# Optimization experiments

Hardware: AMD Instinct MI355X
Metric: run time of the kernel (lower is better)

Reference implementation:

```python
import jax, jax.numpy as jnp
import numpy as np
from jax import lax

H = 50; W = 50; C = 512; A = 9; P = 3; K = 2048; NC = 20
DIN = C * P * P  # 4608, flattened ROI-pooled feature


def _conv(x, w, b):
    # x [N,H,W,Cin], w [kh,kw,Cin,Cout]
    return lax.conv_general_dilated(x, w, (1, 1), 'SAME',
                                    dimension_numbers=('NHWC', 'HWIO', 'NHWC')) + b


def _roi_align(feat, boxes):
    # feat [H,W,C]; boxes [K,4] = (x1,x2,y1,y2) in feature-map coords -> [K,P,P,C]
    Hf, Wf, _ = feat.shape
    t = (jnp.arange(P, dtype=feat.dtype) + 0.5) / P
    xs = boxes[:, 0:1] + (boxes[:, 1:2] - boxes[:, 0:1]) * t  # [K,P]
    ys = boxes[:, 2:3] + (boxes[:, 3:4] - boxes[:, 2:3]) * t  # [K,P]
    x0f = jnp.floor(xs); y0f = jnp.floor(ys)
    fx = (xs - x0f)[:, None, :, None]  # [K,1,P,1]
    fy = (ys - y0f)[:, :, None, None]  # [K,P,1,1]
    x0 = jnp.clip(x0f.astype(jnp.int32), 0, Wf - 1); x1i = jnp.clip(x0 + 1, 0, Wf - 1)
    y0 = jnp.clip(y0f.astype(jnp.int32), 0, Hf - 1); y1i = jnp.clip(y0 + 1, 0, Hf - 1)

    def g(yi, xi):  # [K,P],[K,P] -> [K,P,P,C]
        return feat[yi[:, :, None], xi[:, None, :]]

    return (g(y0, x0) * (1 - fy) * (1 - fx) + g(y0, x1i) * (1 - fy) * fx
            + g(y1i, x0) * fy * (1 - fx) + g(y1i, x1i) * fy * fx)


def setup_inputs() -> dict:
    key = jax.random.key(0)
    ks = jax.random.split(key, 16)

    def w(k, shape, fan_in):
        return jax.random.normal(k, shape, jnp.float32) / np.float32(np.sqrt(fan_in))

    return {
        'features': jax.random.normal(ks[0], (1, H, W, C), jnp.float32),
        'labels': jax.random.randint(ks[1], (NC,), 0, 2, dtype=jnp.int32),
        'rpn_w': w(ks[2], (2, 2, C, C), 4 * C), 'rpn_b': jnp.zeros((C,), jnp.float32),
        'cls_w': w(ks[3], (1, 1, C, A), C), 'cls_b': jnp.zeros((A,), jnp.float32),
        'reg_w': w(ks[4], (1, 1, C, 4 * A), C), 'reg_b': jnp.zeros((4 * A,), jnp.float32),
        'fc6_w': w(ks[5], (DIN, 9216), DIN), 'fc6_b': jnp.zeros((9216,), jnp.float32),
        'fc7_w': w(ks[6], (9216, 4096), 9216), 'fc7_b': jnp.zeros((4096,), jnp.float32),
        'fc8c_w': w(ks[7], (4096, NC), 4096), 'fc8c_b': jnp.zeros((NC,), jnp.float32),
        'fc8d_w': w(ks[8], (4096, NC), 4096), 'fc8d_b': jnp.zeros((NC,), jnp.float32),
    }


def reference(features, labels, rpn_w, rpn_b, cls_w, cls_b, reg_w, reg_b,
              fc6_w, fc6_b, fc7_w, fc7_b, fc8c_w, fc8c_b, fc8d_w, fc8d_b):
    # RPN head
    x = jax.nn.relu(_conv(features, rpn_w, rpn_b))
    obj = jax.nn.sigmoid(_conv(x, cls_w, cls_b))  # [1,H,W,A] objectness
    reg = _conv(x, reg_w, reg_b)
    # Objectness filtering: fixed-size top-K replaces dynamic threshold filter
    _, idx = lax.top_k(obj.reshape(-1), K)
    raw = reg.reshape(-1, 4)[idx]                 # [K,4]
    s = jax.nn.sigmoid(raw)
    Wd = jnp.float32(W); Hd = jnp.float32(H)
    x1 = s[:, 0] * (Wd - 2.0); x2 = x1 + 1.0 + s[:, 1] * (Wd - 1.0 - x1)
    y1 = s[:, 2] * (Hd - 2.0); y2 = y1 + 1.0 + s[:, 3] * (Hd - 1.0 - y1)
    # original slices feature map with integer coords -> non-differentiable
    boxes = lax.stop_gradient(jnp.stack([x1, x2, y1, y2], axis=1))  # [K,4]
    # Per-ROI pooling (vectorized ROI-align)
    pooled = _roi_align(features[0], boxes).reshape(K, -1)  # [K,DIN]
    # FC trunk + two-stream WSDDN head
    h = jax.nn.relu(pooled @ fc6_w + fc6_b)
    h = jax.nn.relu(h @ fc7_w + fc7_b)
    c = jax.nn.softmax(h @ fc8c_w + fc8c_b, axis=0)  # softmax over regions
    d = jax.nn.softmax(h @ fc8d_w + fc8d_b, axis=1)  # softmax over classes
    scores = c * d                                   # [K,NC]
    output = jnp.clip(jnp.sum(scores, axis=0), 0.0, 1.0)  # [NC]
    return output, scores, boxes
```

## Files before the change

kernel.cpp:

```cpp
#include <hip/hip_runtime.h>
#include <math.h>


#define HN 50
#define WN 50
#define CN 512
#define AN 9
#define KTOP 2048
#define NCL 20
#define NOBJ 22500

typedef unsigned short ushort_t;
typedef __attribute__((ext_vector_type(8))) short short8;
typedef __attribute__((ext_vector_type(4))) float floatx4;

__device__ __forceinline__ ushort_t bf16_rne(float f) {
    unsigned int u = __float_as_uint(f);
    unsigned int r = (u + 0x7FFFu + ((u >> 16) & 1u)) >> 16;
    return (ushort_t)r;
}

__device__ __forceinline__ void gl_lds16(const void* g, void* l) {
    __builtin_amdgcn_global_load_lds(
        (const __attribute__((address_space(1))) unsigned int*)g,
        (__attribute__((address_space(3))) unsigned int*)l, 16, 0, 0);
}

__launch_bounds__(256)
__global__ void conv_chain_kernel(const float* __restrict__ feat,
                                  const float* __restrict__ rpnw,
                                  const float* __restrict__ rpnb,
                                  float* __restrict__ x32)
{
    __shared__ float xs[16 * 512];
    const int tid = threadIdx.x;
    const int hwBase = blockIdx.x * 4;
    const int co = blockIdx.y * 256 + tid;

    for (int t = tid; t < 16 * 512; t += 256) {
        int slot = t >> 9, c = t & 511;
        int hwL = slot >> 2, tap = slot & 3;
        int hw = hwBase + hwL;
        int h = hw / WN, w = hw % WN;
        int hy = h + (tap >> 1), wx = w + (tap & 1);
        float v = 0.f;
        if (hy < HN && wx < WN) v = feat[(size_t)(hy * WN + wx) * CN + c];
        xs[t] = v;
    }
    __syncthreads();

    float acc[4][4];
#pragma unroll
    for (int i = 0; i < 4; i++)
#pragma unroll
        for (int t = 0; t < 4; t++) acc[i][t] = 0.f;

    for (int c = 0; c < CN; c++) {
        float wv0 = rpnw[(size_t)(0 * CN + c) * CN + co];
        float wv1 = rpnw[(size_t)(1 * CN + c) * CN + co];
        float wv2 = rpnw[(size_t)(2 * CN + c) * CN + co];
        float wv3 = rpnw[(size_t)(3 * CN + c) * CN + co];
#pragma unroll
        for (int i = 0; i < 4; i++) {
            acc[i][0] = fmaf(xs[(i * 4 + 0) * 512 + c], wv0, acc[i][0]);
            acc[i][1] = fmaf(xs[(i * 4 + 1) * 512 + c], wv1, acc[i][1]);
            acc[i][2] = fmaf(xs[(i * 4 + 2) * 512 + c], wv2, acc[i][2]);
            acc[i][3] = fmaf(xs[(i * 4 + 3) * 512 + c], wv3, acc[i][3]);
        }
    }
    float b = rpnb[co];
#pragma unroll
    for (int i = 0; i < 4; i++) {
        float v = ((acc[i][0] + acc[i][1]) + acc[i][2]) + acc[i][3];
        v = v + b;
        v = v > 0.f ? v : 0.f;
        x32[(size_t)(hwBase + i) * CN + co] = v;
    }
}

__launch_bounds__(256)
__global__ void obj_chain_kernel(const float* __restrict__ x32,
                                 const float* __restrict__ clsw,
                                 const float* __restrict__ clsb,
                                 float* __restrict__ key)
{
    int i = blockIdx.x * 256 + threadIdx.x;
    if (i >= NOBJ) return;
    int hw = i / AN, a = i % AN;
    const float* xr = x32 + (size_t)hw * CN;
    float acc = 0.f;
    for (int c = 0; c < CN; c++) acc = fmaf(xr[c], clsw[c * AN + a], acc);
    float l32 = acc + clsb[a];
    float s32 = (float)(1.0 / (1.0 + exp(-(double)l32)));
    key[i] = s32;
}

__launch_bounds__(256)
__global__ void topk_count_kernel(const float* __restrict__ key, int* __restrict__ cnt)
{
    __shared__ float ch[2048];
    int tid = threadIdx.x;
    int j0 = blockIdx.y * 2048;
    for (int t = tid; t < 2048; t += 256) {
        int jg = j0 + t;
        ch[t] = (jg < NOBJ) ? key[jg] : -1.0f;
    }
    int i = blockIdx.x * 256 + tid;
    float vi = (i < NOBJ) ? key[i] : 2.0f;
    __syncthreads();
    int c = 0;
    for (int t = 0; t < 2048; t++) {
        float vj = ch[t];
        int jg = j0 + t;
        c += (vj > vi || (vj == vi && jg < i)) ? 1 : 0;
    }
    if (i < NOBJ && c) atomicAdd(&cnt[i], c);
}

__launch_bounds__(256)
__global__ void topk_scatter_kernel(const int* __restrict__ cnt, int* __restrict__ sorted)
{
    int i = blockIdx.x * 256 + threadIdx.x;
    if (i < NOBJ) {
        int r = cnt[i];
        if (r < KTOP) sorted[r] = i;
    }
}

__launch_bounds__(256)
__global__ void boxes_kernel(const int* __restrict__ sorted,
                             const float* __restrict__ x32,
                             const float* __restrict__ regw,
                             const float* __restrict__ regb,
                             double* __restrict__ boxd,
                             float* __restrict__ outBoxes)
{
    int k = blockIdx.x * 256 + threadIdx.x;
    if (k >= KTOP) return;
    int i = sorted[k];
    int hw = i / AN, a = i % AN;
    const float* xr = x32 + (size_t)hw * CN;
    float r0 = 0.f, r1 = 0.f, r2 = 0.f, r3 = 0.f;
    for (int c = 0; c < CN; c++) {
        float xv = xr[c];
        const float* wr = regw + (size_t)c * (4 * AN) + 4 * a;
        r0 = fmaf(xv, wr[0], r0);
        r1 = fmaf(xv, wr[1], r1);
        r2 = fmaf(xv, wr[2], r2);
        r3 = fmaf(xv, wr[3], r3);
    }
    r0 = r0 + regb[4 * a + 0];
    r1 = r1 + regb[4 * a + 1];
    r2 = r2 + regb[4 * a + 2];
    r3 = r3 + regb[4 * a + 3];
    double s0 = 1.0 / (1.0 + exp(-(double)r0));
    double s1 = 1.0 / (1.0 + exp(-(double)r1));
    double s2 = 1.0 / (1.0 + exp(-(double)r2));
    double s3 = 1.0 / (1.0 + exp(-(double)r3));
    double x1 = s0 * (double)(WN - 2);
    double x2 = x1 + 1.0 + s1 * ((double)(WN - 1) - x1);
    double y1 = s2 * (double)(HN - 2);
    double y2 = y1 + 1.0 + s3 * ((double)(HN - 1) - y1);
    boxd[4 * k + 0] = x1; boxd[4 * k + 1] = x2;
    boxd[4 * k + 2] = y1; boxd[4 * k + 3] = y2;
    outBoxes[4 * k + 0] = (float)x1; outBoxes[4 * k + 1] = (float)x2;
    outBoxes[4 * k + 2] = (float)y1; outBoxes[4 * k + 3] = (float)y2;
}

__launch_bounds__(256)
__global__ void roi_kernel(const float* __restrict__ feat,
                           const double* __restrict__ boxd,
                           ushort_t* __restrict__ pooled)
{
    int k = blockIdx.x;
    int tid = threadIdx.x;
    double x1 = boxd[4 * k + 0], x2 = boxd[4 * k + 1];
    double y1 = boxd[4 * k + 2], y2 = boxd[4 * k + 3];
    int ix0[3], ix1[3], iy0[3], iy1[3];
    double fx[3], fy[3];
#pragma unroll
    for (int p = 0; p < 3; p++) {
        double t = ((double)p + 0.5) / 3.0;
        double xsv = x1 + (x2 - x1) * t;
        double x0f = floor(xsv);
        fx[p] = xsv - x0f;
        int xi = (int)x0f;
        xi = xi < 0 ? 0 : (xi > WN - 1 ? WN - 1 : xi);
        ix0[p] = xi;
        ix1[p] = (xi + 1 > WN - 1) ? WN - 1 : xi + 1;
        double ysv = y1 + (y2 - y1) * t;
        double y0f = floor(ysv);
        fy[p] = ysv - y0f;
        int yi = (int)y0f;
        yi = yi < 0 ? 0 : (yi > HN - 1 ? HN - 1 : yi);
        iy0[p] = yi;
        iy1[p] = (yi + 1 > HN - 1) ? HN - 1 : yi + 1;
    }
#pragma unroll
    for (int pp = 0; pp < 9; pp++) {
        int py = pp / 3, px = pp % 3;
        double w00 = (1.0 - fy[py]) * (1.0 - fx[px]);
        double w01 = (1.0 - fy[py]) * fx[px];
        double w10 = fy[py] * (1.0 - fx[px]);
        double w11 = fy[py] * fx[px];
        const float* f00 = feat + (size_t)(iy0[py] * WN + ix0[px]) * CN;
        const float* f01 = feat + (size_t)(iy0[py] * WN + ix1[px]) * CN;
        const float* f10 = feat + (size_t)(iy1[py] * WN + ix0[px]) * CN;
        const float* f11 = feat + (size_t)(iy1[py] * WN + ix1[px]) * CN;
        ushort_t* dst = pooled + ((size_t)k * 9 + pp) * CN;
        for (int c = tid; c < CN; c += 256) {
            double v = w00 * (double)f00[c] + w01 * (double)f01[c]
                     + w10 * (double)f10[c] + w11 * (double)f11[c];
            dst[c] = bf16_rne((float)v);
        }
    }
}

__launch_bounds__(256)
__global__ void transpose_cvt_kernel(const float* __restrict__ W,
                                     ushort_t* __restrict__ Wt,
                                     int K, int N, int n0)
{
    __shared__ float tile[64][65];
    const int tid = threadIdx.x;
    const int k0 = blockIdx.x * 64;
    const int nb = blockIdx.y * 64;
#pragma unroll
    for (int q = 0; q < 4; q++) {
        int r = (tid >> 4) + q * 16;
        int c = (tid & 15) * 4;
        float4 v = *(const float4*)&W[(size_t)(k0 + r) * N + n0 + nb + c];
        tile[r][c + 0] = v.x; tile[r][c + 1] = v.y;
        tile[r][c + 2] = v.z; tile[r][c + 3] = v.w;
    }
    __syncthreads();
#pragma unroll
    for (int q = 0; q < 4; q++) {
        int rn = (tid >> 4) + q * 16;
        int ck = (tid & 15) * 4;
        ushort4 o;
        o.x = bf16_rne(tile[ck + 0][rn]);
        o.y = bf16_rne(tile[ck + 1][rn]);
        o.z = bf16_rne(tile[ck + 2][rn]);
        o.w = bf16_rne(tile[ck + 3][rn]);
        *(ushort4*)&Wt[(size_t)(nb + rn) * K + k0 + ck] = o;
    }
}

__launch_bounds__(256)
__global__ void pack_w8_kernel(const float* __restrict__ cw,
                               const float* __restrict__ dw,
                               ushort_t* __restrict__ Wt8)
{
    int idx = blockIdx.x * 256 + threadIdx.x;
    int n = idx >> 12, k = idx & 4095;
    float v = 0.f;
    if (n < NCL) v = cw[(size_t)k * NCL + n];
    else if (n < 2 * NCL) v = dw[(size_t)k * NCL + (n - NCL)];
    Wt8[(size_t)n * 4096 + k] = bf16_rne(v);
}

__launch_bounds__(128)
__global__ void pack_b8_kernel(const float* __restrict__ cb,
                               const float* __restrict__ db,
                               float* __restrict__ b8)
{
    int n = threadIdx.x;
    float v = 0.f;
    if (n < NCL) v = cb[n];
    else if (n < 2 * NCL) v = db[n - NCL];
    b8[n] = v;
}

template <bool OUT_BF16, bool RELU>
__launch_bounds__(256)
__global__ void gemm_bt_kernel(const ushort_t* __restrict__ A,
                               const ushort_t* __restrict__ Bt,
                               const float* __restrict__ bias,
                               void* __restrict__ Cv,
                               int Nc, int K)
{
    __shared__ ushort_t As[128 * 32];
    __shared__ ushort_t Bs[128 * 32];
    const int tid = threadIdx.x;
    const int w = tid >> 6, l = tid & 63;
    const int mBase = blockIdx.y * 128, nBase = blockIdx.x * 128;
    const int mW = (w >> 1) * 64, nW = (w & 1) * 64;

    floatx4 acc[4][4];
#pragma unroll
    for (int i = 0; i < 4; i++)
#pragma unroll
        for (int j = 0; j < 4; j++) acc[i][j] = (floatx4){0.f, 0.f, 0.f, 0.f};

    const int r0 = tid >> 2;
    const int ce = (tid & 3) * 8;

    for (int kb = 0; kb < K; kb += 32) {
        __syncthreads();
        gl_lds16(&A[(size_t)(mBase + r0) * K + kb + ce], &As[tid * 8]);
        gl_lds16(&A[(size_t)(mBase + r0 + 64) * K + kb + ce], &As[2048 + tid * 8]);
        gl_lds16(&Bt[(size_t)(nBase + r0) * K + kb + ce], &Bs[tid * 8]);
        gl_lds16(&Bt[(size_t)(nBase + r0 + 64) * K + kb + ce], &Bs[2048 + tid * 8]);
        __syncthreads();

        short8 aF[4], bF[4];
#pragma unroll
        for (int i = 0; i < 4; i++)
            aF[i] = *(const short8*)&As[(mW + i * 16 + (l & 15)) * 32 + (l >> 4) * 8];
#pragma unroll
        for (int j = 0; j < 4; j++)
            bF[j] = *(const short8*)&Bs[(nW + j * 16 + (l & 15)) * 32 + (l >> 4) * 8];
#pragma unroll
        for (int i = 0; i < 4; i++)
#pragma unroll
            for (int j = 0; j < 4; j++)
                acc[i][j] = __builtin_amdgcn_mfma_f32_16x16x32_bf16(aF[i], bF[j], acc[i][j], 0, 0, 0);
    }

#pragma unroll
    for (int i = 0; i < 4; i++) {
        int rowT = mBase + mW + i * 16 + (l >> 4) * 4;
#pragma unroll
        for (int j = 0; j < 4; j++) {
            int col = nBase + nW + j * 16 + (l & 15);
            float bv = bias[col];
#pragma unroll
            for (int r = 0; r < 4; r++) {
                float v = acc[i][j][r] + bv;
                if (RELU) v = v > 0.f ? v : 0.f;
                size_t idx = (size_t)(rowT + r) * Nc + col;
                if (OUT_BF16) ((ushort_t*)Cv)[idx] = bf16_rne(v);
                else ((float*)Cv)[idx] = v;
            }
        }
    }
}

__launch_bounds__(256)
__global__ void colstats_kernel(const float* __restrict__ logits,
                                double* __restrict__ cmax, double* __restrict__ csum)
{
    __shared__ double red[4];
    int j = blockIdx.x, tid = threadIdx.x;
    double m = -1.0e300;
    for (int i = tid; i < KTOP; i += 256) m = fmax(m, (double)logits[(size_t)i * 128 + j]);
    for (int off = 32; off > 0; off >>= 1) m = fmax(m, __shfl_down(m, off, 64));
    if ((tid & 63) == 0) red[tid >> 6] = m;
    __syncthreads();
    double mm = fmax(fmax(red[0], red[1]), fmax(red[2], red[3]));
    __syncthreads();
    double s = 0.0;
    for (int i = tid; i < KTOP; i += 256) s += exp((double)logits[(size_t)i * 128 + j] - mm);
    for (int off = 32; off > 0; off >>= 1) s += __shfl_down(s, off, 64);
    if ((tid & 63) == 0) red[tid >> 6] = s;
    __syncthreads();
    if (tid == 0) { cmax[j] = mm; csum[j] = red[0] + red[1] + red[2] + red[3]; }
}

__launch_bounds__(256)
__global__ void scores_kernel(const float* __restrict__ logits,
                              const double* __restrict__ cmax, const double* __restrict__ csum,
                              double* __restrict__ scd, float* __restrict__ outScores)
{
    int i = blockIdx.x * 256 + threadIdx.x;
    if (i >= KTOP) return;
    const float* lr = logits + (size_t)i * 128;
    double rm = -1.0e300;
#pragma unroll
    for (int j = 0; j < NCL; j++) rm = fmax(rm, (double)lr[NCL + j]);
    double rs = 0.0;
#pragma unroll
    for (int j = 0; j < NCL; j++) rs += exp((double)lr[NCL + j] - rm);
#pragma unroll
    for (int j = 0; j < NCL; j++) {
        double cc = exp((double)lr[j] - cmax[j]) / csum[j];
        double dd = exp((double)lr[NCL + j] - rm) / rs;
        double sc = cc * dd;
        scd[(size_t)i * NCL + j] = sc;
        outScores[(size_t)i * NCL + j] = (float)sc;
    }
}

__launch_bounds__(256)
__global__ void colsum_kernel(const double* __restrict__ scd, float* __restrict__ out)
{
    __shared__ double red[4];
    int j = blockIdx.x, tid = threadIdx.x;
    double s = 0.0;
    for (int i = tid; i < KTOP; i += 256) s += scd[(size_t)i * NCL + j];
    for (int off = 32; off > 0; off >>= 1) s += __shfl_down(s, off, 64);
    if ((tid & 63) == 0) red[tid >> 6] = s;
    __syncthreads();
    if (tid == 0) {
        double t = red[0] + red[1] + red[2] + red[3];
        t = t < 0.0 ? 0.0 : (t > 1.0 ? 1.0 : t);
        out[j] = (float)t;
    }
}

extern "C" void kernel_launch(void* const* d_in, const int* in_sizes, int n_in,
                              void* d_out, int out_size, void* d_ws, size_t ws_size,
                              hipStream_t stream)
{
    const float* features = (const float*)d_in[0];
    const float* rpn_w  = (const float*)d_in[2];
    const float* rpn_b  = (const float*)d_in[3];
    const float* cls_w  = (const float*)d_in[4];
    const float* cls_b  = (const float*)d_in[5];
    const float* reg_w  = (const float*)d_in[6];
    const float* reg_b  = (const float*)d_in[7];
    const float* fc6_w  = (const float*)d_in[8];
    const float* fc6_b  = (const float*)d_in[9];
    const float* fc7_w  = (const float*)d_in[10];
    const float* fc7_b  = (const float*)d_in[11];
    const float* fc8c_w = (const float*)d_in[12];
    const float* fc8c_b = (const float*)d_in[13];
    const float* fc8d_w = (const float*)d_in[14];
    const float* fc8d_b = (const float*)d_in[15];

    float* out = (float*)d_out;
    char* ws = (char*)d_ws;

    const size_t OFF_H6   = 0;
    const size_t OFF_WT   = 37748736;
    const size_t OFF_ABF  = 80216064;
    const size_t OFF_H7   = 80216064;
    const size_t OFF_X32  = 0;
    const size_t OFF_KEY  = 5120000;
    const size_t OFF_CNT  = 5210112;
    const size_t OFF_SORT = 5300224;
    const size_t OFF_BOXD = 5308416;
    const size_t OFF_LOGIT = OFF_WT + 37748736;
    const size_t OFF_W8T   = OFF_LOGIT + 1048576;
    const size_t OFF_B8    = OFF_W8T + 1048576;
    const size_t OFF_SCD   = OFF_B8 + 512;
    const size_t OFF_CMAX  = OFF_SCD + 327680;
    const size_t OFF_CSUM  = OFF_CMAX + 512;

    float*    x32    = (float*)(ws + OFF_X32);
    float*    key    = (float*)(ws + OFF_KEY);
    int*      cnt    = (int*)(ws + OFF_CNT);
    int*      sorted = (int*)(ws + OFF_SORT);
    double*   boxd   = (double*)(ws + OFF_BOXD);
    ushort_t* Abf    = (ushort_t*)(ws + OFF_ABF);
    ushort_t* Wt     = (ushort_t*)(ws + OFF_WT);
    ushort_t* h6bf   = (ushort_t*)(ws + OFF_H6);
    ushort_t* h7bf   = (ushort_t*)(ws + OFF_H7);
    float*    logits = (float*)(ws + OFF_LOGIT);
    ushort_t* Wt8    = (ushort_t*)(ws + OFF_W8T);
    float*    b8     = (float*)(ws + OFF_B8);
    double*   scd    = (double*)(ws + OFF_SCD);
    double*   cmax   = (double*)(ws + OFF_CMAX);
    double*   csum   = (double*)(ws + OFF_CSUM);

    float* outScores = out + NCL;
    float* outBoxes  = out + NCL + KTOP * NCL;

    conv_chain_kernel<<<dim3(625, 2), 256, 0, stream>>>(features, rpn_w, rpn_b, x32);
    obj_chain_kernel<<<dim3(88), 256, 0, stream>>>(x32, cls_w, cls_b, key);
    hipMemsetAsync(cnt, 0, NOBJ * sizeof(int), stream);
    topk_count_kernel<<<dim3(88, 11), 256, 0, stream>>>(key, cnt);
    topk_scatter_kernel<<<dim3(88), 256, 0, stream>>>(cnt, sorted);
    boxes_kernel<<<dim3(8), 256, 0, stream>>>(sorted, x32, reg_w, reg_b, boxd, outBoxes);

    roi_kernel<<<dim3(KTOP), 256, 0, stream>>>(features, boxd, Abf);

    transpose_cvt_kernel<<<dim3(72, 72), 256, 0, stream>>>(fc6_w, Wt, 4608, 9216, 0);
    gemm_bt_kernel<true, true><<<dim3(36, 16), 256, 0, stream>>>(Abf, Wt, fc6_b + 0,
                                                                 (void*)(h6bf + 0), 9216, 4608);
    transpose_cvt_kernel<<<dim3(72, 72), 256, 0, stream>>>(fc6_w, Wt, 4608, 9216, 4608);
    gemm_bt_kernel<true, true><<<dim3(36, 16), 256, 0, stream>>>(Abf, Wt, fc6_b + 4608,
                                                                 (void*)(h6bf + 4608), 9216, 4608);

    transpose_cvt_kernel<<<dim3(144, 32), 256, 0, stream>>>(fc7_w, Wt, 9216, 4096, 0);
    gemm_bt_kernel<true, true><<<dim3(16, 16), 256, 0, stream>>>(h6bf, Wt, fc7_b + 0,
                                                                 (void*)(h7bf + 0), 4096, 9216);
    transpose_cvt_kernel<<<dim3(144, 32), 256, 0, stream>>>(fc7_w, Wt, 9216, 4096, 2048);
    gemm_bt_kernel<true, true><<<dim3(16, 16), 256, 0, stream>>>(h6bf, Wt, fc7_b + 2048,
                                                                 (void*)(h7bf + 2048), 4096, 9216);

    pack_w8_kernel<<<dim3(2048), 256, 0, stream>>>(fc8c_w, fc8d_w, Wt8);
    pack_b8_kernel<<<dim3(1), 128, 0, stream>>>(fc8c_b, fc8d_b, b8);
    gemm_bt_kernel<false, false><<<dim3(1, 16), 256, 0, stream>>>(h7bf, Wt8, b8,
                                                                  (void*)logits, 128, 4096);

    colstats_kernel<<<dim3(NCL), 256, 0, stream>>>(logits, cmax, csum);
    scores_kernel<<<dim3(8), 256, 0, stream>>>(logits, cmax, csum, scd, outScores);
    colsum_kernel<<<dim3(NCL), 256, 0, stream>>>(scd, out);
}
```

Before: 1.598 ms.

## Double-buffer GEMM LDS loads, swizzle tiles across XCDs, drop conv LDS staging

The bf16 GEMM kernel now double-buffers its LDS tiles, issuing the next k-slice's global-to-LDS loads before running the MFMAs on the current one, so each iteration needs one barrier instead of two. It also remaps workgroup ids so neighbouring tiles land on the same XCD for better L2 reuse, and changes the LDS layout to k-chunk-major. The RPN conv kernel drops its shared-memory staging and instead reads float4 feature vectors straight from global memory, using a zero row in place of out-of-bounds taps. The trade-offs are twice the GEMM LDS footprint, more registers in the conv kernel, and heavier reliance on cache for the conv input loads.

```diff
diff --git a/kernel.cpp b/kernel.cpp
--- a/kernel.cpp
+++ b/kernel.cpp
@@ -14,6 +14,8 @@
 typedef __attribute__((ext_vector_type(8))) short short8;
 typedef __attribute__((ext_vector_type(4))) float floatx4;
 
+__device__ float conv_zero_row[CN];
+
 __device__ __forceinline__ ushort_t bf16_rne(float f) {
     unsigned int u = __float_as_uint(f);
     unsigned int r = (u + 0x7FFFu + ((u >> 16) & 1u)) >> 16;
@@ -32,22 +34,23 @@
                                   const float* __restrict__ rpnb,
                                   float* __restrict__ x32)
 {
-    __shared__ float xs[16 * 512];
     const int tid = threadIdx.x;
     const int hwBase = blockIdx.x * 4;
     const int co = blockIdx.y * 256 + tid;
 
-    for (int t = tid; t < 16 * 512; t += 256) {
-        int slot = t >> 9, c = t & 511;
-        int hwL = slot >> 2, tap = slot & 3;
-        int hw = hwBase + hwL;
+    const float* rp[4][4];
+#pragma unroll
+    for (int i = 0; i < 4; i++) {
+        int hw = hwBase + i;
         int h = hw / WN, w = hw % WN;
-        int hy = h + (tap >> 1), wx = w + (tap & 1);
-        float v = 0.f;
-        if (hy < HN && wx < WN) v = feat[(size_t)(hy * WN + wx) * CN + c];
-        xs[t] = v;
-    }
-    __syncthreads();
+#pragma unroll
+        for (int t = 0; t < 4; t++) {
+            int hy = h + (t >> 1), wx = w + (t & 1);
+            rp[i][t] = (hy < HN && wx < WN)
+                           ? feat + (size_t)(hy * WN + wx) * CN
+                           : conv_zero_row;
+        }
+    }
 
     float acc[4][4];
 #pragma unroll
@@ -55,19 +58,32 @@
 #pragma unroll
         for (int t = 0; t < 4; t++) acc[i][t] = 0.f;
 
-    for (int c = 0; c < CN; c++) {
-        float wv0 = rpnw[(size_t)(0 * CN + c) * CN + co];
-        float wv1 = rpnw[(size_t)(1 * CN + c) * CN + co];
-        float wv2 = rpnw[(size_t)(2 * CN + c) * CN + co];
-        float wv3 = rpnw[(size_t)(3 * CN + c) * CN + co];
-#pragma unroll
-        for (int i = 0; i < 4; i++) {
-            acc[i][0] = fmaf(xs[(i * 4 + 0) * 512 + c], wv0, acc[i][0]);
-            acc[i][1] = fmaf(xs[(i * 4 + 1) * 512 + c], wv1, acc[i][1]);
-            acc[i][2] = fmaf(xs[(i * 4 + 2) * 512 + c], wv2, acc[i][2]);
-            acc[i][3] = fmaf(xs[(i * 4 + 3) * 512 + c], wv3, acc[i][3]);
+    for (int cq = 0; cq < CN; cq += 4) {
+        float4 xv[4][4];
+#pragma unroll
+        for (int i = 0; i < 4; i++)
+#pragma unroll
+            for (int t = 0; t < 4; t++)
+                xv[i][t] = *(const float4*)(rp[i][t] + cq);
+
+#pragma unroll
+        for (int cc = 0; cc < 4; cc++) {
+            float wv[4];
+#pragma unroll
+            for (int t = 0; t < 4; t++)
+                wv[t] = rpnw[(size_t)(t * CN + cq + cc) * CN + co];
+#pragma unroll
+            for (int i = 0; i < 4; i++)
+#pragma unroll
+                for (int t = 0; t < 4; t++) {
+                    float xvv = cc == 0 ? xv[i][t].x
+                              : cc == 1 ? xv[i][t].y
+                              : cc == 2 ? xv[i][t].z : xv[i][t].w;
+                    acc[i][t] = fmaf(xvv, wv[t], acc[i][t]);
+                }
         }
     }
+
     float b = rpnb[co];
 #pragma unroll
     for (int i = 0; i < 4; i++) {
@@ -272,6 +288,16 @@
     b8[n] = v;
 }
 
+#define GEMM_STAGE(buf, kb)                                                              \
+    gl_lds16(&A[(size_t)(mBase + (tid & 127)) * K + (kb) + (tid >> 7) * 8],              \
+             &As[buf][tid * 8]);                                                         \
+    gl_lds16(&A[(size_t)(mBase + (tid & 127)) * K + (kb) + ((tid >> 7) + 2) * 8],        \
+             &As[buf][(256 + tid) * 8]);                                                 \
+    gl_lds16(&Bt[(size_t)(nBase + (tid & 127)) * K + (kb) + (tid >> 7) * 8],             \
+             &Bs[buf][tid * 8]);                                                         \
+    gl_lds16(&Bt[(size_t)(nBase + (tid & 127)) * K + (kb) + ((tid >> 7) + 2) * 8],       \
+             &Bs[buf][(256 + tid) * 8]);
+
 template <bool OUT_BF16, bool RELU>
 __launch_bounds__(256)
 __global__ void gemm_bt_kernel(const ushort_t* __restrict__ A,
@@ -280,11 +306,18 @@
                                void* __restrict__ Cv,
                                int Nc, int K)
 {
-    __shared__ ushort_t As[128 * 32];
-    __shared__ ushort_t Bs[128 * 32];
+    __shared__ ushort_t As[2][128 * 32];
+    __shared__ ushort_t Bs[2][128 * 32];
     const int tid = threadIdx.x;
     const int w = tid >> 6, l = tid & 63;
-    const int mBase = blockIdx.y * 128, nBase = blockIdx.x * 128;
+
+    const int nwg = gridDim.x * gridDim.y;
+    const int hwid = blockIdx.y * gridDim.x + blockIdx.x;
+    const int q = nwg >> 3, r = nwg & 7;
+    const int xcd = hwid & 7, i0 = hwid >> 3;
+    const int swz = (xcd < r ? xcd * (q + 1) : r * (q + 1) + (xcd - r) * q) + i0;
+    const int nBase = (swz / gridDim.y) * 128;
+    const int mBase = (swz % gridDim.y) * 128;
     const int mW = (w >> 1) * 64, nW = (w & 1) * 64;
 
     floatx4 acc[4][4];
@@ -293,29 +326,30 @@
 #pragma unroll
         for (int j = 0; j < 4; j++) acc[i][j] = (floatx4){0.f, 0.f, 0.f, 0.f};
 
-    const int r0 = tid >> 2;
-    const int ce = (tid & 3) * 8;
-
+    GEMM_STAGE(0, 0);
+    asm volatile("s_waitcnt vmcnt(0)" ::: "memory");
+    __syncthreads();
+
+    int cur = 0;
     for (int kb = 0; kb < K; kb += 32) {
-        __syncthreads();
-        gl_lds16(&A[(size_t)(mBase + r0) * K + kb + ce], &As[tid * 8]);
-        gl_lds16(&A[(size_t)(mBase + r0 + 64) * K + kb + ce], &As[2048 + tid * 8]);
-        gl_lds16(&Bt[(size_t)(nBase + r0) * K + kb + ce], &Bs[tid * 8]);
-        gl_lds16(&Bt[(size_t)(nBase + r0 + 64) * K + kb + ce], &Bs[2048 + tid * 8]);
-        __syncthreads();
+        if (kb + 32 < K) { GEMM_STAGE(cur ^ 1, kb + 32); }
 
         short8 aF[4], bF[4];
 #pragma unroll
         for (int i = 0; i < 4; i++)
-            aF[i] = *(const short8*)&As[(mW + i * 16 + (l & 15)) * 32 + (l >> 4) * 8];
+            aF[i] = *(const short8*)&As[cur][((l >> 4) * 128 + mW + i * 16 + (l & 15)) * 8];
 #pragma unroll
         for (int j = 0; j < 4; j++)
-            bF[j] = *(const short8*)&Bs[(nW + j * 16 + (l & 15)) * 32 + (l >> 4) * 8];
+            bF[j] = *(const short8*)&Bs[cur][((l >> 4) * 128 + nW + j * 16 + (l & 15)) * 8];
 #pragma unroll
         for (int i = 0; i < 4; i++)
 #pragma unroll
             for (int j = 0; j < 4; j++)
                 acc[i][j] = __builtin_amdgcn_mfma_f32_16x16x32_bf16(aF[i], bF[j], acc[i][j], 0, 0, 0);
+
+        asm volatile("s_waitcnt vmcnt(0)" ::: "memory");
+        __syncthreads();
+        cur ^= 1;
     }
 
 #pragma unroll
@@ -326,10 +360,10 @@
             int col = nBase + nW + j * 16 + (l & 15);
             float bv = bias[col];
 #pragma unroll
-            for (int r = 0; r < 4; r++) {
-                float v = acc[i][j][r] + bv;
+            for (int r2 = 0; r2 < 4; r2++) {
+                float v = acc[i][j][r2] + bv;
                 if (RELU) v = v > 0.f ? v : 0.f;
-                size_t idx = (size_t)(rowT + r) * Nc + col;
+                size_t idx = (size_t)(rowT + r2) * Nc + col;
                 if (OUT_BF16) ((ushort_t*)Cv)[idx] = bf16_rne(v);
                 else ((float*)Cv)[idx] = v;
             }
```

Result: slower. 1.867 ms (+16.8%).
